# Performance work log

Measured on AMD Instinct MI355X. Metric: run time of the kernel, lower is better.

## Reference

```python
import jax, jax.numpy as jnp
import numpy as np


def setup_inputs() -> dict:
    key = jax.random.key(0)
    k_x, k_pos, k_val, k_temp = jax.random.split(key, 4)
    B, T, D, N = 8, 2048, 512, 4096
    x = jax.random.normal(k_x, (B, T, D), dtype=jnp.float32)
    # module init: positions ~ N(0,1)*0.5, values ~ N(0,1)*0.02
    positions = jax.random.normal(k_pos, (N, D), dtype=jnp.float32) * 0.5
    values = jax.random.normal(k_val, (N, D), dtype=jnp.float32) * 0.02
    # 'trained' temperatures ~ U[4,6] so the RBF kernel does not underflow at D=512
    temperature = 4.0 + 2.0 * jax.random.uniform(k_temp, (N,), dtype=jnp.float32)
    # neuron_scale buffer at late-tide level (MAX_SCALE = 0.8)
    neuron_scale = jnp.full((N,), 0.8, dtype=jnp.float32)
    return {"x": x, "positions": positions, "values": values,
            "temperature": temperature, "neuron_scale": neuron_scale}


def reference(x, positions, values, temperature, neuron_scale):
    B, T, D = x.shape
    x_flat = x.reshape(-1, D)                                  # [M, D], M = B*T
    x_sq = jnp.sum(x_flat * x_flat, axis=-1, keepdims=True)    # [M, 1]
    p_sq = jnp.sum(positions * positions, axis=-1)             # [N]
    cross = x_flat @ positions.T                               # [M, N] GEMM
    dists = jnp.sqrt(jnp.maximum(x_sq + p_sq[None, :] - 2.0 * cross, 0.0))
    effective_temp = (jnp.abs(temperature) + 0.1) * neuron_scale  # [N]
    weights = jnp.exp(-dists / effective_temp[None, :])        # [M, N]
    weights = weights / (jnp.sum(weights, axis=-1, keepdims=True) + 1e-8)
    out = weights @ values                                     # [M, D] GEMM
    return out.reshape(B, T, D)
```

## Files before the change

kernel.cpp:

```cpp
#include <hip/hip_runtime.h>
#include <hip/hip_bf16.h>

typedef __attribute__((ext_vector_type(8))) short short8;
typedef __attribute__((ext_vector_type(4))) float f32x4;
typedef __attribute__((ext_vector_type(4))) unsigned short u16x4;

__device__ __forceinline__ unsigned short f2bf(float f) {
  union { float f; unsigned u; } v; v.f = f;
  unsigned r = v.u + 0x7fffu + ((v.u >> 16) & 1u);
  return (unsigned short)(r >> 16);
}

template <int EPI, int WM, int WN, int MI, int BK, int NBUF>
__global__ __launch_bounds__(WM * WN * 64, 4) void rbf_gemm(
    const unsigned short* __restrict__ A, const unsigned short* __restrict__ Bt,
    int Ncols, int K,
    const float* __restrict__ xsq, const float* __restrict__ psq,
    const float* __restrict__ rtemp, unsigned short* __restrict__ Wout,
    float* __restrict__ part, int Mtot, const float* __restrict__ denin,
    float* __restrict__ outp, int row0, int ldOut) {
  constexpr int NT = WM * WN * 64;
  constexpr int BM = WM * MI * 16;
  constexpr int BN = WN * 64;
  constexpr int CH = BK / 8;
  constexpr int CMASK = CH - 1;
  constexpr int AIT = BM * CH / NT;
  constexpr int BIT = BN * CH / NT;
  constexpr int LOADS = AIT + BIT;
  constexpr int KS = BK / 32;
  constexpr int ASZ = BM * BK;
  constexpr int TSZ = (BM + BN) * BK;
  constexpr int BOUNCE = EPI == 1 ? BM * BN * 2 : BM * BN;
  constexpr int SELEMS = NBUF * TSZ > BOUNCE ? NBUF * TSZ : BOUNCE;
  __shared__ __align__(16) unsigned short smem[SELEMS];

  const int t = threadIdx.x;
  const int lane = t & 63, wid = t >> 6;
  const int wm = wid / WN, wn = wid % WN;
  const int lr = lane & 15, lg = lane >> 4;

  const int nbm = gridDim.x / (Ncols / BN);
  const int bm = blockIdx.x % nbm;
  const int bn = blockIdx.x / nbm;

  const unsigned short* Ab = A + (size_t)bm * BM * K;
  const unsigned short* Bb = Bt + (size_t)bn * BN * K;

  const unsigned short* gA[AIT];
  const unsigned short* gB[BIT];
#pragma unroll
  for (int i = 0; i < AIT; ++i) {
    const int idx = i * NT + t;
    const int r = idx / CH, c = idx & CMASK;
    gA[i] = Ab + (size_t)r * K + ((c ^ (r & CMASK)) << 3);
  }
#pragma unroll
  for (int i = 0; i < BIT; ++i) {
    const int idx = i * NT + t;
    const int r = idx / CH, c = idx & CMASK;
    gB[i] = Bb + (size_t)r * K + ((c ^ (r & CMASK)) << 3);
  }
  const int dwave = wid << 9;

  int offA[MI][KS], offB[4][KS];
#pragma unroll
  for (int mi = 0; mi < MI; ++mi) {
    const int ar = wm * (MI * 16) + mi * 16 + lr;
#pragma unroll
    for (int ks = 0; ks < KS; ++ks)
      offA[mi][ks] = ar * BK + ((((ks << 2) | lg) ^ (ar & CMASK)) << 3);
  }
#pragma unroll
  for (int ni = 0; ni < 4; ++ni) {
    const int br = wn * 64 + ni * 16 + lr;
#pragma unroll
    for (int ks = 0; ks < KS; ++ks)
      offB[ni][ks] = ASZ + br * BK + ((((ks << 2) | lg) ^ (br & CMASK)) << 3);
  }

  f32x4 acc[MI][4];
#pragma unroll
  for (int i = 0; i < MI; ++i)
#pragma unroll
    for (int j = 0; j < 4; ++j) acc[i][j] = (f32x4){0.f, 0.f, 0.f, 0.f};

#define STAGE(bo)                                                                      \
  do {                                                                                 \
    _Pragma("unroll")                                                                  \
    for (int i = 0; i < AIT; ++i) {                                                    \
      __builtin_amdgcn_global_load_lds(                                                \
          (const __attribute__((address_space(1))) void*)gA[i],                        \
          (__attribute__((address_space(3))) void*)(smem + (bo) + i * (NT * 8) + dwave), \
          16, 0, 0);                                                                   \
      gA[i] += BK;                                                                     \
    }                                                                                  \
    _Pragma("unroll")                                                                  \
    for (int i = 0; i < BIT; ++i) {                                                    \
      __builtin_amdgcn_global_load_lds(                                                \
          (const __attribute__((address_space(1))) void*)gB[i],                        \
          (__attribute__((address_space(3))) void*)(smem + (bo) + ASZ + i * (NT * 8) + dwave), \
          16, 0, 0);                                                                   \
      gB[i] += BK;                                                                     \
    }                                                                                  \
  } while (0)

  const int nsteps = K / BK;
#pragma unroll
  for (int p = 0; p < NBUF - 1; ++p)
    if (p < nsteps) STAGE(p * TSZ);

  int bc = 0, bp = (NBUF - 1) % NBUF;
  for (int s = 0; s < nsteps; ++s) {
    if (s + NBUF - 1 < nsteps) {
      STAGE(bp * TSZ);
      asm volatile("s_waitcnt vmcnt(%0)" :: "i"((NBUF - 1) * LOADS) : "memory");
    } else if (NBUF >= 3 && s + 1 < nsteps) {
      asm volatile("s_waitcnt vmcnt(%0)" :: "i"(LOADS) : "memory");
    } else {
      asm volatile("s_waitcnt vmcnt(0)" ::: "memory");
    }
    __builtin_amdgcn_s_barrier();
    const unsigned short* sb = smem + bc * TSZ;
    __builtin_amdgcn_s_setprio(1);
#pragma unroll
    for (int ks = 0; ks < KS; ++ks) {
      short8 af[MI], bf[4];
#pragma unroll
      for (int mi = 0; mi < MI; ++mi) af[mi] = *(const short8*)&sb[offA[mi][ks]];
#pragma unroll
      for (int ni = 0; ni < 4; ++ni) bf[ni] = *(const short8*)&sb[offB[ni][ks]];
#pragma unroll
      for (int mi = 0; mi < MI; ++mi)
#pragma unroll
        for (int ni = 0; ni < 4; ++ni)
          acc[mi][ni] = __builtin_amdgcn_mfma_f32_16x16x32_bf16(af[mi], bf[ni],
                                                                acc[mi][ni], 0, 0, 0);
    }
    __builtin_amdgcn_s_setprio(0);
    asm volatile("s_waitcnt lgkmcnt(0)" ::: "memory");
    __builtin_amdgcn_s_barrier();
    bc = bc + 1 == NBUF ? 0 : bc + 1;
    bp = bp + 1 == NBUF ? 0 : bp + 1;
  }
#undef STAGE

  if (EPI == 0) {
    float ps[4], rt[4];
#pragma unroll
    for (int ni = 0; ni < 4; ++ni) {
      const int col = bn * BN + wn * 64 + ni * 16 + lr;
      ps[ni] = psq[col];
      rt[ni] = rtemp[col];
    }
    float* slice = part + (size_t)(bn * WN + wn) * Mtot;
#pragma unroll
    for (int mi = 0; mi < MI; ++mi) {
#pragma unroll
      for (int j = 0; j < 4; ++j) {
        const int lrow = wm * (MI * 16) + mi * 16 + lg * 4 + j;
        const int grow = row0 + bm * BM + lrow;
        const float xq = xsq[grow];
        float rsv = 0.f;
#pragma unroll
        for (int ni = 0; ni < 4; ++ni) {
          const int lcol = wn * 64 + ni * 16 + lr;
          float d2 = xq + ps[ni] - 2.0f * acc[mi][ni][j];
          float dist = __builtin_amdgcn_sqrtf(fmaxf(d2, 0.0f));
          float w = __builtin_amdgcn_exp2f(-dist * rt[ni]);
          smem[lrow * BN + (((lcol >> 3) ^ (lrow & 7)) << 3) + (lcol & 7)] = f2bf(w);
          rsv += w;
        }
        rsv += __shfl_xor(rsv, 1);
        rsv += __shfl_xor(rsv, 2);
        rsv += __shfl_xor(rsv, 4);
        rsv += __shfl_xor(rsv, 8);
        if (lr == 0) slice[grow] = rsv;
      }
    }
    __syncthreads();
    constexpr int HB = BN / 8;
#pragma unroll
    for (int i = 0; i < BM * BN / 8 / NT; ++i) {
      const int id = i * NT + t;
      const int r = id / HB, h = id % HB;
      short8 v = *(const short8*)&smem[r * BN + ((h ^ (r & 7)) << 3)];
      *(short8*)&Wout[(size_t)(bm * BM + r) * ldOut + bn * BN + h * 8] = v;
    }
  } else {
    float* smemf = (float*)smem;
#pragma unroll
    for (int mi = 0; mi < MI; ++mi)
#pragma unroll
      for (int j = 0; j < 4; ++j) {
        const int lrow = wm * (MI * 16) + mi * 16 + lg * 4 + j;
#pragma unroll
        for (int ni = 0; ni < 4; ++ni) {
          const int lcol = wn * 64 + ni * 16 + lr;
          smemf[lrow * BN + (((lcol >> 2) ^ (lrow & 7)) << 2) + (lcol & 3)] =
              acc[mi][ni][j];
        }
      }
    __syncthreads();
    constexpr int HB4 = BN / 4;
#pragma unroll
    for (int i = 0; i < BM * BN / 4 / NT; ++i) {
      const int id = i * NT + t;
      const int r = id / HB4, h = id % HB4;
      const int grow = row0 + bm * BM + r;
      const float rd = 1.0f / (denin[grow] + 1e-8f);
      f32x4 v = *(const f32x4*)&smemf[r * BN + ((h ^ (r & 7)) << 2)];
      v *= rd;
      __builtin_nontemporal_store(v,
          (f32x4*)&outp[(size_t)grow * ldOut + bn * BN + h * 4]);
    }
  }
}

__global__ void reduce_denom(const float* __restrict__ part, float* __restrict__ denom,
                             int Mtot, int row0, int S) {
  const int m = row0 + blockIdx.x * 128 + threadIdx.x;
  float s = 0.f;
  for (int i = 0; i < S; ++i) s += part[(size_t)i * Mtot + m];
  denom[m] = s;
}

__global__ void prep_rows2(const float* __restrict__ x, const float* __restrict__ pos,
                           unsigned short* __restrict__ xb, unsigned short* __restrict__ pb,
                           float* __restrict__ xsq, float* __restrict__ psq,
                           int D, int M) {
  const int row = blockIdx.x;
  const float* in;
  unsigned short* outb;
  float* sq;
  int r;
  if (row < M) {
    in = x; outb = xb; sq = xsq; r = row;
  } else {
    in = pos; outb = pb; sq = psq; r = row - M;
  }
  const int t = threadIdx.x;
  const float4 v = ((const float4*)(in + (size_t)r * D))[t];
  u16x4 o = {f2bf(v.x), f2bf(v.y), f2bf(v.z), f2bf(v.w)};
  *(u16x4*)(outb + (size_t)r * D + t * 4) = o;
  float s = v.x * v.x + v.y * v.y + v.z * v.z + v.w * v.w;
  for (int off = 32; off; off >>= 1) s += __shfl_xor(s, off);
  __shared__ float ws[16];
  if ((t & 63) == 0) ws[t >> 6] = s;
  __syncthreads();
  if (t == 0) {
    float tot = 0.f;
    const int nw = blockDim.x >> 6;
    for (int i = 0; i < nw; ++i) tot += ws[i];
    sq[r] = tot;
  }
}

__global__ void prep_scale(const float* __restrict__ tmp, const float* __restrict__ sc,
                           float* __restrict__ rtemp, int N) {
  const int i = blockIdx.x * blockDim.x + threadIdx.x;
  if (i < N) rtemp[i] = 1.4426950408889634f / ((fabsf(tmp[i]) + 0.1f) * sc[i]);
}

__global__ void prep_vT(const float* __restrict__ vals, unsigned short* __restrict__ vT,
                        int N, int D) {
  __shared__ float tile[32][33];
  const int nt = blockIdx.x, dt = blockIdx.y;
  const int tx = threadIdx.x, ty = threadIdx.y;
#pragma unroll
  for (int i = 0; i < 4; ++i) {
    int r = nt * 32 + ty + i * 8;
    tile[ty + i * 8][tx] = vals[(size_t)r * D + dt * 32 + tx];
  }
  __syncthreads();
#pragma unroll
  for (int i = 0; i < 4; ++i) {
    int d = dt * 32 + ty + i * 8;
    vT[(size_t)d * N + nt * 32 + tx] = f2bf(tile[tx][ty + i * 8]);
  }
}

extern "C" void kernel_launch(void* const* d_in, const int* in_sizes, int n_in,
                              void* d_out, int out_size, void* d_ws, size_t ws_size,
                              hipStream_t stream) {
  const float* x = (const float*)d_in[0];
  const float* pos = (const float*)d_in[1];
  const float* vals = (const float*)d_in[2];
  const float* temp = (const float*)d_in[3];
  const float* nsc = (const float*)d_in[4];
  float* out = (float*)d_out;

  const int N = in_sizes[3];
  const int D = in_sizes[1] / N;
  const int M = in_sizes[0] / D;
  const int S = 4 * (N / 256);

  char* ws = (char*)d_ws;
  size_t off = 0;
  auto alloc = [&](size_t bytes) {
    void* p = ws + off;
    off = (off + bytes + 255) & ~(size_t)255;
    return p;
  };
  unsigned short* xb = (unsigned short*)alloc((size_t)M * D * 2);
  unsigned short* pb = (unsigned short*)alloc((size_t)N * D * 2);
  unsigned short* vT = (unsigned short*)alloc((size_t)D * N * 2);
  float* xsq = (float*)alloc((size_t)M * 4);
  float* psq = (float*)alloc((size_t)N * 4);
  float* rtemp = (float*)alloc((size_t)N * 4);
  float* denom = (float*)alloc((size_t)M * 4);
  float* part = (float*)alloc((size_t)S * M * 4);

  size_t avail = ws_size > off ? ws_size - off : 0;
  long long mc_ll = (long long)(avail / ((size_t)N * 2));
  int Mc = (int)((mc_ll / 128) * 128);
  if (Mc > M) Mc = M;
  if (Mc < 128) Mc = 128;
  unsigned short* W = (unsigned short*)alloc((size_t)Mc * N * 2);

  prep_rows2<<<M + N, D / 4, 0, stream>>>(x, pos, xb, pb, xsq, psq, D, M);
  prep_scale<<<(N + 255) / 256, 256, 0, stream>>>(temp, nsc, rtemp, N);
  dim3 tg(N / 32, D / 32);
  prep_vT<<<tg, dim3(32, 8), 0, stream>>>(vals, vT, N, D);

  for (int row0 = 0; row0 < M; row0 += Mc) {
    const int mc = (M - row0) < Mc ? (M - row0) : Mc;
    const int g1 = (mc / 128) * (N / 256);
    rbf_gemm<0, 2, 4, 4, 32, 3><<<g1, 512, 0, stream>>>(
        xb + (size_t)row0 * D, pb, N, D, xsq, psq, rtemp, W, part, M,
        nullptr, nullptr, row0, N);
    reduce_denom<<<mc / 128, 128, 0, stream>>>(part, denom, M, row0, S);
    const int g2 = (mc / 128) * (D / 256);
    rbf_gemm<1, 2, 4, 4, 64, 2><<<g2, 512, 0, stream>>>(
        W, vT, D, N, nullptr, nullptr, nullptr, nullptr,
        part, M, denom, out, row0, D);
  }
}
```

Measured before the change: 205.9 us.

## Use 32x32x16 MFMA kernel for distance GEMM and simplify pipeline to double buffering

Replaces the first GEMM (x·positionsᵀ with RBF epilogue) with a dedicated kernel using 32x32x16 bf16 MFMA tiles, 2x2 fragments per wave and double-buffered LDS staging. The 16x16x32 MFMA tiles and the triple-buffered pipeline are dropped. The larger MFMA shape is meant to cut LDS fragment reads per FLOP and raise matrix-core efficiency. The second GEMM keeps its template but its pipeline becomes a fixed two-stage ping-pong, which is equivalent for its NBUF=2 config. Epilogue row mapping and the reduction are adapted to the 32x32 accumulator layout (shuffle over 32 lanes).

```diff
diff --git a/kernel.cpp b/kernel.cpp
--- a/kernel.cpp
+++ b/kernel.cpp
@@ -3,6 +3,7 @@
 
 typedef __attribute__((ext_vector_type(8))) short short8;
 typedef __attribute__((ext_vector_type(4))) float f32x4;
+typedef __attribute__((ext_vector_type(16))) float f32x16;
 typedef __attribute__((ext_vector_type(4))) unsigned short u16x4;
 
 __device__ __forceinline__ unsigned short f2bf(float f) {
@@ -11,13 +12,167 @@
   return (unsigned short)(r >> 16);
 }
 
-template <int EPI, int WM, int WN, int MI, int BK, int NBUF>
-__global__ __launch_bounds__(WM * WN * 64, 4) void rbf_gemm(
+#define GLL(src, dst)                                                     \
+  __builtin_amdgcn_global_load_lds(                                       \
+      (const __attribute__((address_space(1))) void*)(src),               \
+      (__attribute__((address_space(3))) void*)(dst), 16, 0, 0)
+#define BAR __builtin_amdgcn_s_barrier()
+
+__global__ __launch_bounds__(512, 4) void rbf_qk32(
     const unsigned short* __restrict__ A, const unsigned short* __restrict__ Bt,
     int Ncols, int K,
     const float* __restrict__ xsq, const float* __restrict__ psq,
     const float* __restrict__ rtemp, unsigned short* __restrict__ Wout,
-    float* __restrict__ part, int Mtot, const float* __restrict__ denin,
+    float* __restrict__ part, int Mtot, int row0, int ldOut) {
+  constexpr int BK = 32;
+  constexpr int ASZ = 128 * 32;
+  constexpr int TSZ = (128 + 256) * 32;
+  __shared__ __align__(16) unsigned short smem[32768];
+
+  const int t = threadIdx.x;
+  const int lane = t & 63, wid = t >> 6;
+  const int wm = wid >> 2, wn = wid & 3;
+  const int l31 = lane & 31, lh = lane >> 5;
+
+  const int nbm = gridDim.x / (Ncols >> 8);
+  const int bm = blockIdx.x % nbm;
+  const int bn = blockIdx.x / nbm;
+
+  const unsigned short* Ab = A + (size_t)bm * 128 * K;
+  const unsigned short* Bb = Bt + (size_t)bn * 256 * K;
+
+  const unsigned short* gA;
+  const unsigned short* gB[2];
+  {
+    const int r = t >> 2, c = t & 3;
+    gA = Ab + (size_t)r * K + ((c ^ (r & 3)) << 3);
+  }
+#pragma unroll
+  for (int i = 0; i < 2; ++i) {
+    const int idx = i * 512 + t;
+    const int r = idx >> 2, c = idx & 3;
+    gB[i] = Bb + (size_t)r * K + ((c ^ (r & 3)) << 3);
+  }
+  const int dwave = wid << 9;
+
+#define STAGE(bo)                                                   \
+  do {                                                              \
+    GLL(gA, smem + (bo) + dwave);                                   \
+    gA += BK;                                                       \
+    GLL(gB[0], smem + (bo) + ASZ + dwave);                          \
+    gB[0] += BK;                                                    \
+    GLL(gB[1], smem + (bo) + ASZ + 4096 + dwave);                   \
+    gB[1] += BK;                                                    \
+  } while (0)
+
+  int offA[2][2], offB[2][2];
+#pragma unroll
+  for (int fi = 0; fi < 2; ++fi) {
+    const int ar = wm * 64 + fi * 32 + l31;
+#pragma unroll
+    for (int ks = 0; ks < 2; ++ks)
+      offA[fi][ks] = ar * 32 + (((2 * ks + lh) ^ (ar & 3)) << 3);
+  }
+#pragma unroll
+  for (int fj = 0; fj < 2; ++fj) {
+    const int br = wn * 64 + fj * 32 + l31;
+#pragma unroll
+    for (int ks = 0; ks < 2; ++ks)
+      offB[fj][ks] = ASZ + br * 32 + (((2 * ks + lh) ^ (br & 3)) << 3);
+  }
+
+  f32x16 acc[2][2];
+#pragma unroll
+  for (int i = 0; i < 2; ++i)
+#pragma unroll
+    for (int j = 0; j < 2; ++j)
+#pragma unroll
+      for (int e = 0; e < 16; ++e) acc[i][j][e] = 0.f;
+
+  const int nsteps = K / BK;
+  STAGE(0);
+  unsigned buf = 0;
+  for (int s = 0; s < nsteps; ++s) {
+    if (s + 1 < nsteps) {
+      STAGE(buf ^ TSZ);
+      asm volatile("s_waitcnt vmcnt(3)" ::: "memory");
+    } else {
+      asm volatile("s_waitcnt vmcnt(0)" ::: "memory");
+    }
+    BAR;
+    const unsigned short* sb = smem + buf;
+    short8 af[2][2], bf[2][2];
+#pragma unroll
+    for (int fi = 0; fi < 2; ++fi)
+#pragma unroll
+      for (int ks = 0; ks < 2; ++ks) af[fi][ks] = *(const short8*)&sb[offA[fi][ks]];
+#pragma unroll
+    for (int fj = 0; fj < 2; ++fj)
+#pragma unroll
+      for (int ks = 0; ks < 2; ++ks) bf[fj][ks] = *(const short8*)&sb[offB[fj][ks]];
+    __builtin_amdgcn_s_setprio(1);
+#pragma unroll
+    for (int ks = 0; ks < 2; ++ks)
+#pragma unroll
+      for (int fi = 0; fi < 2; ++fi)
+#pragma unroll
+        for (int fj = 0; fj < 2; ++fj)
+          acc[fi][fj] = __builtin_amdgcn_mfma_f32_32x32x16_bf16(
+              af[fi][ks], bf[fj][ks], acc[fi][fj], 0, 0, 0);
+    __builtin_amdgcn_s_setprio(0);
+    asm volatile("s_waitcnt lgkmcnt(0)" ::: "memory");
+    BAR;
+    buf ^= TSZ;
+  }
+#undef STAGE
+
+  float ps_[2], rt_[2];
+#pragma unroll
+  for (int fj = 0; fj < 2; ++fj) {
+    const int col = bn * 256 + wn * 64 + fj * 32 + l31;
+    ps_[fj] = psq[col];
+    rt_[fj] = rtemp[col];
+  }
+  float* slice = part + (size_t)(bn * 4 + wn) * Mtot;
+#pragma unroll
+  for (int fi = 0; fi < 2; ++fi) {
+#pragma unroll
+    for (int r = 0; r < 16; ++r) {
+      const int lrow = wm * 64 + fi * 32 + (r & 3) + 8 * (r >> 2) + 4 * lh;
+      const int grow = row0 + bm * 128 + lrow;
+      const float xq = xsq[grow];
+      float rsv = 0.f;
+#pragma unroll
+      for (int fj = 0; fj < 2; ++fj) {
+        const int lcol = wn * 64 + fj * 32 + l31;
+        float d2 = xq + ps_[fj] - 2.0f * acc[fi][fj][r];
+        float dist = __builtin_amdgcn_sqrtf(fmaxf(d2, 0.0f));
+        float w = __builtin_amdgcn_exp2f(-dist * rt_[fj]);
+        smem[lrow * 256 + (((lcol >> 3) ^ (lrow & 7)) << 3) + (lcol & 7)] = f2bf(w);
+        rsv += w;
+      }
+      rsv += __shfl_xor(rsv, 1);
+      rsv += __shfl_xor(rsv, 2);
+      rsv += __shfl_xor(rsv, 4);
+      rsv += __shfl_xor(rsv, 8);
+      rsv += __shfl_xor(rsv, 16);
+      if (l31 == 0) slice[grow] = rsv;
+    }
+  }
+  __syncthreads();
+#pragma unroll
+  for (int i = 0; i < 8; ++i) {
+    const int id = i * 512 + t;
+    const int r = id >> 5, h = id & 31;
+    short8 v = *(const short8*)&smem[r * 256 + ((h ^ (r & 7)) << 3)];
+    *(short8*)&Wout[(size_t)(bm * 128 + r) * ldOut + bn * 256 + h * 8] = v;
+  }
+}
+
+template <int EPI, int WM, int WN, int MI, int BK, int NBUF>
+__global__ __launch_bounds__(WM * WN * 64, 4) void rbf_gemm(
+    const unsigned short* __restrict__ A, const unsigned short* __restrict__ Bt,
+    int Ncols, int K, const float* __restrict__ denin,
     float* __restrict__ outp, int row0, int ldOut) {
   constexpr int NT = WM * WN * 64;
   constexpr int BM = WM * MI * 16;
@@ -30,7 +185,7 @@
   constexpr int KS = BK / 32;
   constexpr int ASZ = BM * BK;
   constexpr int TSZ = (BM + BN) * BK;
-  constexpr int BOUNCE = EPI == 1 ? BM * BN * 2 : BM * BN;
+  constexpr int BOUNCE = BM * BN * 2;
   constexpr int SELEMS = NBUF * TSZ > BOUNCE ? NBUF * TSZ : BOUNCE;
   __shared__ __align__(16) unsigned short smem[SELEMS];
 
@@ -84,43 +239,30 @@
 #pragma unroll
     for (int j = 0; j < 4; ++j) acc[i][j] = (f32x4){0.f, 0.f, 0.f, 0.f};
 
-#define STAGE(bo)                                                                      \
-  do {                                                                                 \
-    _Pragma("unroll")                                                                  \
-    for (int i = 0; i < AIT; ++i) {                                                    \
-      __builtin_amdgcn_global_load_lds(                                                \
-          (const __attribute__((address_space(1))) void*)gA[i],                        \
-          (__attribute__((address_space(3))) void*)(smem + (bo) + i * (NT * 8) + dwave), \
-          16, 0, 0);                                                                   \
-      gA[i] += BK;                                                                     \
-    }                                                                                  \
-    _Pragma("unroll")                                                                  \
-    for (int i = 0; i < BIT; ++i) {                                                    \
-      __builtin_amdgcn_global_load_lds(                                                \
-          (const __attribute__((address_space(1))) void*)gB[i],                        \
-          (__attribute__((address_space(3))) void*)(smem + (bo) + ASZ + i * (NT * 8) + dwave), \
-          16, 0, 0);                                                                   \
-      gB[i] += BK;                                                                     \
-    }                                                                                  \
+#define STAGE(bo)                                                              \
+  do {                                                                         \
+    _Pragma("unroll") for (int i = 0; i < AIT; ++i) {                          \
+      GLL(gA[i], smem + (bo) + i * (NT * 8) + dwave);                          \
+      gA[i] += BK;                                                             \
+    }                                                                          \
+    _Pragma("unroll") for (int i = 0; i < BIT; ++i) {                          \
+      GLL(gB[i], smem + (bo) + ASZ + i * (NT * 8) + dwave);                    \
+      gB[i] += BK;                                                             \
+    }                                                                          \
   } while (0)
 
   const int nsteps = K / BK;
-#pragma unroll
-  for (int p = 0; p < NBUF - 1; ++p)
-    if (p < nsteps) STAGE(p * TSZ);
-
-  int bc = 0, bp = (NBUF - 1) % NBUF;
+  STAGE(0);
+  unsigned buf = 0;
   for (int s = 0; s < nsteps; ++s) {
-    if (s + NBUF - 1 < nsteps) {
-      STAGE(bp * TSZ);
-      asm volatile("s_waitcnt vmcnt(%0)" :: "i"((NBUF - 1) * LOADS) : "memory");
-    } else if (NBUF >= 3 && s + 1 < nsteps) {
+    if (s + 1 < nsteps) {
+      STAGE(buf ^ TSZ);
       asm volatile("s_waitcnt vmcnt(%0)" :: "i"(LOADS) : "memory");
     } else {
       asm volatile("s_waitcnt vmcnt(0)" ::: "memory");
     }
-    __builtin_amdgcn_s_barrier();
-    const unsigned short* sb = smem + bc * TSZ;
+    BAR;
+    const unsigned short* sb = smem + buf;
     __builtin_amdgcn_s_setprio(1);
 #pragma unroll
     for (int ks = 0; ks < KS; ++ks) {
@@ -138,81 +280,36 @@
     }
     __builtin_amdgcn_s_setprio(0);
     asm volatile("s_waitcnt lgkmcnt(0)" ::: "memory");
-    __builtin_amdgcn_s_barrier();
-    bc = bc + 1 == NBUF ? 0 : bc + 1;
-    bp = bp + 1 == NBUF ? 0 : bp + 1;
+    BAR;
+    buf ^= TSZ;
   }
 #undef STAGE
 
-  if (EPI == 0) {
-    float ps[4], rt[4];
-#pragma unroll
-    for (int ni = 0; ni < 4; ++ni) {
-      const int col = bn * BN + wn * 64 + ni * 16 + lr;
-      ps[ni] = psq[col];
-      rt[ni] = rtemp[col];
-    }
-    float* slice = part + (size_t)(bn * WN + wn) * Mtot;
-#pragma unroll
-    for (int mi = 0; mi < MI; ++mi) {
-#pragma unroll
-      for (int j = 0; j < 4; ++j) {
-        const int lrow = wm * (MI * 16) + mi * 16 + lg * 4 + j;
-        const int grow = row0 + bm * BM + lrow;
-        const float xq = xsq[grow];
-        float rsv = 0.f;
-#pragma unroll
-        for (int ni = 0; ni < 4; ++ni) {
-          const int lcol = wn * 64 + ni * 16 + lr;
-          float d2 = xq + ps[ni] - 2.0f * acc[mi][ni][j];
-          float dist = __builtin_amdgcn_sqrtf(fmaxf(d2, 0.0f));
-          float w = __builtin_amdgcn_exp2f(-dist * rt[ni]);
-          smem[lrow * BN + (((lcol >> 3) ^ (lrow & 7)) << 3) + (lcol & 7)] = f2bf(w);
-          rsv += w;
-        }
-        rsv += __shfl_xor(rsv, 1);
-        rsv += __shfl_xor(rsv, 2);
-        rsv += __shfl_xor(rsv, 4);
-        rsv += __shfl_xor(rsv, 8);
-        if (lr == 0) slice[grow] = rsv;
+  float* smemf = (float*)smem;
+#pragma unroll
+  for (int mi = 0; mi < MI; ++mi)
+#pragma unroll
+    for (int j = 0; j < 4; ++j) {
+      const int lrow = wm * (MI * 16) + mi * 16 + lg * 4 + j;
+#pragma unroll
+      for (int ni = 0; ni < 4; ++ni) {
+        const int lcol = wn * 64 + ni * 16 + lr;
+        smemf[lrow * BN + (((lcol >> 2) ^ (lrow & 7)) << 2) + (lcol & 3)] =
+            acc[mi][ni][j];
       }
     }
-    __syncthreads();
-    constexpr int HB = BN / 8;
-#pragma unroll
-    for (int i = 0; i < BM * BN / 8 / NT; ++i) {
-      const int id = i * NT + t;
-      const int r = id / HB, h = id % HB;
-      short8 v = *(const short8*)&smem[r * BN + ((h ^ (r & 7)) << 3)];
-      *(short8*)&Wout[(size_t)(bm * BM + r) * ldOut + bn * BN + h * 8] = v;
-    }
-  } else {
-    float* smemf = (float*)smem;
-#pragma unroll
-    for (int mi = 0; mi < MI; ++mi)
-#pragma unroll
-      for (int j = 0; j < 4; ++j) {
-        const int lrow = wm * (MI * 16) + mi * 16 + lg * 4 + j;
-#pragma unroll
-        for (int ni = 0; ni < 4; ++ni) {
-          const int lcol = wn * 64 + ni * 16 + lr;
-          smemf[lrow * BN + (((lcol >> 2) ^ (lrow & 7)) << 2) + (lcol & 3)] =
-              acc[mi][ni][j];
-        }
-      }
-    __syncthreads();
-    constexpr int HB4 = BN / 4;
-#pragma unroll
-    for (int i = 0; i < BM * BN / 4 / NT; ++i) {
-      const int id = i * NT + t;
-      const int r = id / HB4, h = id % HB4;
-      const int grow = row0 + bm * BM + r;
-      const float rd = 1.0f / (denin[grow] + 1e-8f);
-      f32x4 v = *(const f32x4*)&smemf[r * BN + ((h ^ (r & 7)) << 2)];
-      v *= rd;
-      __builtin_nontemporal_store(v,
-          (f32x4*)&outp[(size_t)grow * ldOut + bn * BN + h * 4]);
-    }
+  __syncthreads();
+  constexpr int HB4 = BN / 4;
+#pragma unroll
+  for (int i = 0; i < BM * BN / 4 / NT; ++i) {
+    const int id = i * NT + t;
+    const int r = id / HB4, h = id % HB4;
+    const int grow = row0 + bm * BM + r;
+    const float rd = 1.0f / (denin[grow] + 1e-8f);
+    f32x4 v = *(const f32x4*)&smemf[r * BN + ((h ^ (r & 7)) << 2)];
+    v *= rd;
+    __builtin_nontemporal_store(v,
+        (f32x4*)&outp[(size_t)grow * ldOut + bn * BN + h * 4]);
   }
 }
 
@@ -325,13 +422,11 @@
   for (int row0 = 0; row0 < M; row0 += Mc) {
     const int mc = (M - row0) < Mc ? (M - row0) : Mc;
     const int g1 = (mc / 128) * (N / 256);
-    rbf_gemm<0, 2, 4, 4, 32, 3><<<g1, 512, 0, stream>>>(
-        xb + (size_t)row0 * D, pb, N, D, xsq, psq, rtemp, W, part, M,
-        nullptr, nullptr, row0, N);
+    rbf_qk32<<<g1, 512, 0, stream>>>(
+        xb + (size_t)row0 * D, pb, N, D, xsq, psq, rtemp, W, part, M, row0, N);
     reduce_denom<<<mc / 128, 128, 0, stream>>>(part, denom, M, row0, S);
     const int g2 = (mc / 128) * (D / 256);
     rbf_gemm<1, 2, 4, 4, 64, 2><<<g2, 512, 0, stream>>>(
-        W, vT, D, N, nullptr, nullptr, nullptr, nullptr,
-        part, M, denom, out, row0, D);
-  }
-}
+        W, vT, D, N, denom, out, row0, D);
+  }
+}
```

Result: slower. 242.8 us (+17.9%).

## Replace XOR-swizzled LDS tiles with 16-row chunk layout and double-buffer first GEMM

Applied to the files above, without the earlier changes.

The LDS tile layout changes from a row-major, XOR-swizzled arrangement to one where each 16-row by 8-element chunk is stored contiguously. Global-to-LDS load addresses and the MFMA fragment offsets are updated to match, so each 16-lane group reads consecutive 16-byte words. The pipeline is simplified to strict double buffering, toggled by XOR on the buffer offset, and the distance GEMM drops from three buffers to two. This aims to remove swizzle address arithmetic and LDS bank conflicts and to cut LDS use, but it gives up one stage of load latency hiding and makes each global load touch 16 different rows with short per-row segments.

```diff
diff --git a/kernel.cpp b/kernel.cpp
--- a/kernel.cpp
+++ b/kernel.cpp
@@ -10,6 +10,12 @@
   unsigned r = v.u + 0x7fffu + ((v.u >> 16) & 1u);
   return (unsigned short)(r >> 16);
 }
+
+#define GLL(src, dst)                                                     \
+  __builtin_amdgcn_global_load_lds(                                       \
+      (const __attribute__((address_space(1))) void*)(src),               \
+      (__attribute__((address_space(3))) void*)(dst), 16, 0, 0)
+#define BAR __builtin_amdgcn_s_barrier()
 
 template <int EPI, int WM, int WN, int MI, int BK, int NBUF>
 __global__ __launch_bounds__(WM * WN * 64, 4) void rbf_gemm(
@@ -23,7 +29,6 @@
   constexpr int BM = WM * MI * 16;
   constexpr int BN = WN * 64;
   constexpr int CH = BK / 8;
-  constexpr int CMASK = CH - 1;
   constexpr int AIT = BM * CH / NT;
   constexpr int BIT = BN * CH / NT;
   constexpr int LOADS = AIT + BIT;
@@ -50,33 +55,29 @@
   const unsigned short* gB[BIT];
 #pragma unroll
   for (int i = 0; i < AIT; ++i) {
-    const int idx = i * NT + t;
-    const int r = idx / CH, c = idx & CMASK;
-    gA[i] = Ab + (size_t)r * K + ((c ^ (r & CMASK)) << 3);
+    const int s = i * NT + t;
+    const int g = s / (16 * CH), c = (s >> 4) % CH, ri = s & 15;
+    gA[i] = Ab + (size_t)(g * 16 + ri) * K + c * 8;
   }
 #pragma unroll
   for (int i = 0; i < BIT; ++i) {
-    const int idx = i * NT + t;
-    const int r = idx / CH, c = idx & CMASK;
-    gB[i] = Bb + (size_t)r * K + ((c ^ (r & CMASK)) << 3);
+    const int s = i * NT + t;
+    const int g = s / (16 * CH), c = (s >> 4) % CH, ri = s & 15;
+    gB[i] = Bb + (size_t)(g * 16 + ri) * K + c * 8;
   }
   const int dwave = wid << 9;
 
   int offA[MI][KS], offB[4][KS];
 #pragma unroll
-  for (int mi = 0; mi < MI; ++mi) {
-    const int ar = wm * (MI * 16) + mi * 16 + lr;
+  for (int mi = 0; mi < MI; ++mi)
 #pragma unroll
     for (int ks = 0; ks < KS; ++ks)
-      offA[mi][ks] = ar * BK + ((((ks << 2) | lg) ^ (ar & CMASK)) << 3);
-  }
-#pragma unroll
-  for (int ni = 0; ni < 4; ++ni) {
-    const int br = wn * 64 + ni * 16 + lr;
+      offA[mi][ks] = ((wm * MI + mi) * CH + ((ks << 2) | lg)) * 128 + lr * 8;
+#pragma unroll
+  for (int ni = 0; ni < 4; ++ni)
 #pragma unroll
     for (int ks = 0; ks < KS; ++ks)
-      offB[ni][ks] = ASZ + br * BK + ((((ks << 2) | lg) ^ (br & CMASK)) << 3);
-  }
+      offB[ni][ks] = ASZ + ((wn * 4 + ni) * CH + ((ks << 2) | lg)) * 128 + lr * 8;
 
   f32x4 acc[MI][4];
 #pragma unroll
@@ -84,43 +85,30 @@
 #pragma unroll
     for (int j = 0; j < 4; ++j) acc[i][j] = (f32x4){0.f, 0.f, 0.f, 0.f};
 
-#define STAGE(bo)                                                                      \
-  do {                                                                                 \
-    _Pragma("unroll")                                                                  \
-    for (int i = 0; i < AIT; ++i) {                                                    \
-      __builtin_amdgcn_global_load_lds(                                                \
-          (const __attribute__((address_space(1))) void*)gA[i],                        \
-          (__attribute__((address_space(3))) void*)(smem + (bo) + i * (NT * 8) + dwave), \
-          16, 0, 0);                                                                   \
-      gA[i] += BK;                                                                     \
-    }                                                                                  \
-    _Pragma("unroll")                                                                  \
-    for (int i = 0; i < BIT; ++i) {                                                    \
-      __builtin_amdgcn_global_load_lds(                                                \
-          (const __attribute__((address_space(1))) void*)gB[i],                        \
-          (__attribute__((address_space(3))) void*)(smem + (bo) + ASZ + i * (NT * 8) + dwave), \
-          16, 0, 0);                                                                   \
-      gB[i] += BK;                                                                     \
-    }                                                                                  \
+#define STAGE(bo)                                                              \
+  do {                                                                         \
+    _Pragma("unroll") for (int i = 0; i < AIT; ++i) {                          \
+      GLL(gA[i], smem + (bo) + i * (NT * 8) + dwave);                          \
+      gA[i] += BK;                                                             \
+    }                                                                          \
+    _Pragma("unroll") for (int i = 0; i < BIT; ++i) {                          \
+      GLL(gB[i], smem + (bo) + ASZ + i * (NT * 8) + dwave);                    \
+      gB[i] += BK;                                                             \
+    }                                                                          \
   } while (0)
 
   const int nsteps = K / BK;
-#pragma unroll
-  for (int p = 0; p < NBUF - 1; ++p)
-    if (p < nsteps) STAGE(p * TSZ);
-
-  int bc = 0, bp = (NBUF - 1) % NBUF;
+  STAGE(0);
+  unsigned buf = 0;
   for (int s = 0; s < nsteps; ++s) {
-    if (s + NBUF - 1 < nsteps) {
-      STAGE(bp * TSZ);
-      asm volatile("s_waitcnt vmcnt(%0)" :: "i"((NBUF - 1) * LOADS) : "memory");
-    } else if (NBUF >= 3 && s + 1 < nsteps) {
+    if (s + 1 < nsteps) {
+      STAGE(buf ^ TSZ);
       asm volatile("s_waitcnt vmcnt(%0)" :: "i"(LOADS) : "memory");
     } else {
       asm volatile("s_waitcnt vmcnt(0)" ::: "memory");
     }
-    __builtin_amdgcn_s_barrier();
-    const unsigned short* sb = smem + bc * TSZ;
+    BAR;
+    const unsigned short* sb = smem + buf;
     __builtin_amdgcn_s_setprio(1);
 #pragma unroll
     for (int ks = 0; ks < KS; ++ks) {
@@ -138,9 +126,8 @@
     }
     __builtin_amdgcn_s_setprio(0);
     asm volatile("s_waitcnt lgkmcnt(0)" ::: "memory");
-    __builtin_amdgcn_s_barrier();
-    bc = bc + 1 == NBUF ? 0 : bc + 1;
-    bp = bp + 1 == NBUF ? 0 : bp + 1;
+    BAR;
+    buf ^= TSZ;
   }
 #undef STAGE
 
@@ -325,7 +312,7 @@
   for (int row0 = 0; row0 < M; row0 += Mc) {
     const int mc = (M - row0) < Mc ? (M - row0) : Mc;
     const int g1 = (mc / 128) * (N / 256);
-    rbf_gemm<0, 2, 4, 4, 32, 3><<<g1, 512, 0, stream>>>(
+    rbf_gemm<0, 2, 4, 4, 32, 2><<<g1, 512, 0, stream>>>(
         xb + (size_t)row0 * D, pb, N, D, xsq, psq, rtemp, W, part, M,
         nullptr, nullptr, row0, N);
     reduce_denom<<<mc / 128, 128, 0, stream>>>(part, denom, M, row0, S);
```

Measured after the change: 246.7 us. 1.2x slower.

## Compute softmax denominator from bf16 weights inside second GEMM, drop reduce kernel

Applied to the files above, without the earlier changes.

The first GEMM epilogue no longer computes per-row partial sums and writes them to a partials buffer. The second GEMM instead sums the bf16 weight fragments it already loads from LDS (only the wn==0 waves) and reduces them across lanes through a small shared-memory stash. This removes the reduce_denom launch and the partials traffic. The prep_scale work is also folded into the row-prep kernel to save a launch. The denominator is now summed over bf16-rounded weights, which matches the rounded weights used in the product, and it adds VALU work inside the MFMA loop for some waves.

```diff
diff --git a/kernel.cpp b/kernel.cpp
--- a/kernel.cpp
+++ b/kernel.cpp
@@ -9,6 +9,12 @@
   union { float f; unsigned u; } v; v.f = f;
   unsigned r = v.u + 0x7fffu + ((v.u >> 16) & 1u);
   return (unsigned short)(r >> 16);
+}
+
+__device__ __forceinline__ float bf2f(short s) {
+  union { unsigned u; float f; } v;
+  v.u = ((unsigned)(unsigned short)s) << 16;
+  return v.f;
 }
 
 template <int EPI, int WM, int WN, int MI, int BK, int NBUF>
@@ -17,7 +23,6 @@
     int Ncols, int K,
     const float* __restrict__ xsq, const float* __restrict__ psq,
     const float* __restrict__ rtemp, unsigned short* __restrict__ Wout,
-    float* __restrict__ part, int Mtot, const float* __restrict__ denin,
     float* __restrict__ outp, int row0, int ldOut) {
   constexpr int NT = WM * WN * 64;
   constexpr int BM = WM * MI * 16;
@@ -31,7 +36,8 @@
   constexpr int ASZ = BM * BK;
   constexpr int TSZ = (BM + BN) * BK;
   constexpr int BOUNCE = EPI == 1 ? BM * BN * 2 : BM * BN;
-  constexpr int SELEMS = NBUF * TSZ > BOUNCE ? NBUF * TSZ : BOUNCE;
+  constexpr int SBASE = NBUF * TSZ > BOUNCE ? NBUF * TSZ : BOUNCE;
+  constexpr int SELEMS = SBASE + (EPI == 1 ? 256 : 0);
   __shared__ __align__(16) unsigned short smem[SELEMS];
 
   const int t = threadIdx.x;
@@ -83,6 +89,9 @@
   for (int i = 0; i < MI; ++i)
 #pragma unroll
     for (int j = 0; j < 4; ++j) acc[i][j] = (f32x4){0.f, 0.f, 0.f, 0.f};
+  float den[MI];
+#pragma unroll
+  for (int i = 0; i < MI; ++i) den[i] = 0.f;
 
 #define STAGE(bo)                                                                      \
   do {                                                                                 \
@@ -135,6 +144,15 @@
         for (int ni = 0; ni < 4; ++ni)
           acc[mi][ni] = __builtin_amdgcn_mfma_f32_16x16x32_bf16(af[mi], bf[ni],
                                                                 acc[mi][ni], 0, 0, 0);
+      if (EPI == 1 && wn == 0) {
+#pragma unroll
+        for (int mi = 0; mi < MI; ++mi) {
+          float d0 = 0.f;
+#pragma unroll
+          for (int e = 0; e < 8; ++e) d0 += bf2f(af[mi][e]);
+          den[mi] += d0;
+        }
+      }
     }
     __builtin_amdgcn_s_setprio(0);
     asm volatile("s_waitcnt lgkmcnt(0)" ::: "memory");
@@ -152,7 +170,6 @@
       ps[ni] = psq[col];
       rt[ni] = rtemp[col];
     }
-    float* slice = part + (size_t)(bn * WN + wn) * Mtot;
 #pragma unroll
     for (int mi = 0; mi < MI; ++mi) {
 #pragma unroll
@@ -160,7 +177,6 @@
         const int lrow = wm * (MI * 16) + mi * 16 + lg * 4 + j;
         const int grow = row0 + bm * BM + lrow;
         const float xq = xsq[grow];
-        float rsv = 0.f;
 #pragma unroll
         for (int ni = 0; ni < 4; ++ni) {
           const int lcol = wn * 64 + ni * 16 + lr;
@@ -168,13 +184,7 @@
           float dist = __builtin_amdgcn_sqrtf(fmaxf(d2, 0.0f));
           float w = __builtin_amdgcn_exp2f(-dist * rt[ni]);
           smem[lrow * BN + (((lcol >> 3) ^ (lrow & 7)) << 3) + (lcol & 7)] = f2bf(w);
-          rsv += w;
         }
-        rsv += __shfl_xor(rsv, 1);
-        rsv += __shfl_xor(rsv, 2);
-        rsv += __shfl_xor(rsv, 4);
-        rsv += __shfl_xor(rsv, 8);
-        if (lr == 0) slice[grow] = rsv;
       }
     }
     __syncthreads();
@@ -187,7 +197,18 @@
       *(short8*)&Wout[(size_t)(bm * BM + r) * ldOut + bn * BN + h * 8] = v;
     }
   } else {
+    float* dstash = (float*)(smem + SBASE);
+    if (wn == 0) {
+#pragma unroll
+      for (int mi = 0; mi < MI; ++mi) {
+        float d = den[mi];
+        d += __shfl_xor(d, 16);
+        d += __shfl_xor(d, 32);
+        if (lg == 0) dstash[wm * (MI * 16) + mi * 16 + lr] = d;
+      }
+    }
     float* smemf = (float*)smem;
+    __syncthreads();
 #pragma unroll
     for (int mi = 0; mi < MI; ++mi)
 #pragma unroll
@@ -207,7 +228,7 @@
       const int id = i * NT + t;
       const int r = id / HB4, h = id % HB4;
       const int grow = row0 + bm * BM + r;
-      const float rd = 1.0f / (denin[grow] + 1e-8f);
+      const float rd = 1.0f / (dstash[r] + 1e-8f);
       f32x4 v = *(const f32x4*)&smemf[r * BN + ((h ^ (r & 7)) << 2)];
       v *= rd;
       __builtin_nontemporal_store(v,
@@ -216,19 +237,19 @@
   }
 }
 
-__global__ void reduce_denom(const float* __restrict__ part, float* __restrict__ denom,
-                             int Mtot, int row0, int S) {
-  const int m = row0 + blockIdx.x * 128 + threadIdx.x;
-  float s = 0.f;
-  for (int i = 0; i < S; ++i) s += part[(size_t)i * Mtot + m];
-  denom[m] = s;
-}
-
-__global__ void prep_rows2(const float* __restrict__ x, const float* __restrict__ pos,
-                           unsigned short* __restrict__ xb, unsigned short* __restrict__ pb,
-                           float* __restrict__ xsq, float* __restrict__ psq,
-                           int D, int M) {
+__global__ void prep_all(const float* __restrict__ x, const float* __restrict__ pos,
+                         const float* __restrict__ temp, const float* __restrict__ nsc,
+                         unsigned short* __restrict__ xb, unsigned short* __restrict__ pb,
+                         float* __restrict__ xsq, float* __restrict__ psq,
+                         float* __restrict__ rtemp, int D, int M, int N) {
   const int row = blockIdx.x;
+  const int t = threadIdx.x;
+  if (row >= M + N) {
+    const int i = (row - (M + N)) * 128 + t;
+    if (i < N)
+      rtemp[i] = 1.4426950408889634f / ((fabsf(temp[i]) + 0.1f) * nsc[i]);
+    return;
+  }
   const float* in;
   unsigned short* outb;
   float* sq;
@@ -238,7 +259,6 @@
   } else {
     in = pos; outb = pb; sq = psq; r = row - M;
   }
-  const int t = threadIdx.x;
   const float4 v = ((const float4*)(in + (size_t)r * D))[t];
   u16x4 o = {f2bf(v.x), f2bf(v.y), f2bf(v.z), f2bf(v.w)};
   *(u16x4*)(outb + (size_t)r * D + t * 4) = o;
@@ -255,12 +275,6 @@
   }
 }
 
-__global__ void prep_scale(const float* __restrict__ tmp, const float* __restrict__ sc,
-                           float* __restrict__ rtemp, int N) {
-  const int i = blockIdx.x * blockDim.x + threadIdx.x;
-  if (i < N) rtemp[i] = 1.4426950408889634f / ((fabsf(tmp[i]) + 0.1f) * sc[i]);
-}
-
 __global__ void prep_vT(const float* __restrict__ vals, unsigned short* __restrict__ vT,
                         int N, int D) {
   __shared__ float tile[32][33];
@@ -292,7 +306,6 @@
   const int N = in_sizes[3];
   const int D = in_sizes[1] / N;
   const int M = in_sizes[0] / D;
-  const int S = 4 * (N / 256);
 
   char* ws = (char*)d_ws;
   size_t off = 0;
@@ -307,8 +320,6 @@
   float* xsq = (float*)alloc((size_t)M * 4);
   float* psq = (float*)alloc((size_t)N * 4);
   float* rtemp = (float*)alloc((size_t)N * 4);
-  float* denom = (float*)alloc((size_t)M * 4);
-  float* part = (float*)alloc((size_t)S * M * 4);
 
   size_t avail = ws_size > off ? ws_size - off : 0;
   long long mc_ll = (long long)(avail / ((size_t)N * 2));
@@ -317,8 +328,8 @@
   if (Mc < 128) Mc = 128;
   unsigned short* W = (unsigned short*)alloc((size_t)Mc * N * 2);
 
-  prep_rows2<<<M + N, D / 4, 0, stream>>>(x, pos, xb, pb, xsq, psq, D, M);
-  prep_scale<<<(N + 255) / 256, 256, 0, stream>>>(temp, nsc, rtemp, N);
+  prep_all<<<M + N + (N + 127) / 128, D / 4, 0, stream>>>(
+      x, pos, temp, nsc, xb, pb, xsq, psq, rtemp, D, M, N);
   dim3 tg(N / 32, D / 32);
   prep_vT<<<tg, dim3(32, 8), 0, stream>>>(vals, vT, N, D);
 
@@ -326,12 +337,11 @@
     const int mc = (M - row0) < Mc ? (M - row0) : Mc;
     const int g1 = (mc / 128) * (N / 256);
     rbf_gemm<0, 2, 4, 4, 32, 3><<<g1, 512, 0, stream>>>(
-        xb + (size_t)row0 * D, pb, N, D, xsq, psq, rtemp, W, part, M,
-        nullptr, nullptr, row0, N);
-    reduce_denom<<<mc / 128, 128, 0, stream>>>(part, denom, M, row0, S);
+        xb + (size_t)row0 * D, pb, N, D, xsq, psq, rtemp, W,
+        nullptr, row0, N);
     const int g2 = (mc / 128) * (D / 256);
     rbf_gemm<1, 2, 4, 4, 64, 2><<<g2, 512, 0, stream>>>(
         W, vT, D, N, nullptr, nullptr, nullptr, nullptr,
-        part, M, denom, out, row0, D);
-  }
-}
+        out, row0, D);
+  }
+}
```

After: 197.6 us (median of 2 runs). 1.04x faster.
